# Kernel tuning notes

Measured on AMD Instinct MI355X. Metric: run time of the kernel, lower is better.

The kernel has to match this reference:

```python
import jax, jax.numpy as jnp
import numpy as np

V, E, U, B, S = 32000, 512, 1024, 16, 128
BN_EPS = 1e-3  # keras BatchNormalization default


def setup_inputs() -> dict:
    key = jax.random.key(0)
    ks = jax.random.split(key, 12)
    w = 0.05  # small init keeps the relu-activated LSTM recurrence stable
    return {
        "inputs": jax.random.randint(ks[0], (B, S), 0, V),
        "enc_hidden": jax.random.normal(ks[1], (B, U), jnp.float32) * 0.1,
        "enc_cell": jax.random.normal(ks[2], (B, U), jnp.float32) * 0.1,
        "emb": jax.random.normal(ks[3], (V, E), jnp.float32) * w,
        "Wx": jax.random.normal(ks[4], (E, 4 * U), jnp.float32) * w,
        "Wh": jax.random.normal(ks[5], (U, 4 * U), jnp.float32) * w,
        "b": jnp.zeros((4 * U,), jnp.float32),
        "gamma": jnp.ones((U,), jnp.float32),
        "beta": jnp.zeros((U,), jnp.float32),
        "mov_mean": jnp.zeros((U,), jnp.float32),
        "mov_var": jnp.ones((U,), jnp.float32),
        "W1": jax.random.normal(ks[6], (U, U), jnp.float32) * w,
        "b1": jnp.zeros((U,), jnp.float32),
        "W2": jax.random.normal(ks[7], (U, V), jnp.float32) * w,
        "b2": jnp.zeros((V,), jnp.float32),
    }


def _lstm_relu(xg, mask, h0, c0, Wh):
    # xg: [S,B,4U] precomputed input gates; mask: [S,B] (mask_zero semantics)
    def step(carry, inp):
        h, c = carry
        g, m = inp
        z = g + h @ Wh  # [B,4U]
        i, f, cc, o = jnp.split(z, 4, axis=-1)  # keras gate order i,f,c,o
        i = jax.nn.sigmoid(i)
        f = jax.nn.sigmoid(f)
        o = jax.nn.sigmoid(o)
        cc = jax.nn.relu(cc)  # activation='relu' on candidate
        c_new = f * c + i * cc
        h_new = o * jax.nn.relu(c_new)  # activation='relu' on output
        m = m[:, None]
        h_new = jnp.where(m, h_new, h)  # masked step: carry state/output
        c_new = jnp.where(m, c_new, c)
        return (h_new, c_new), h_new

    (_, _), hs = jax.lax.scan(step, (h0, c0), (xg, mask))
    return hs  # [S,B,U]


def reference(inputs, enc_hidden, enc_cell, emb, Wx, Wh, b, gamma, beta,
              mov_mean, mov_var, W1, b1, W2, b2):
    x = emb[inputs]                       # [B,S,E]
    mask = (inputs != 0)                  # mask_zero=True
    xg = jnp.einsum("bse,eg->bsg", x, Wx) + b   # [B,S,4U]
    hs = _lstm_relu(xg.transpose(1, 0, 2), mask.T, enc_hidden, enc_cell, Wh)
    h = hs.transpose(1, 0, 2)             # [B,S,U]
    # BatchNorm (inference: moving statistics), Dropout is identity at inference
    hbn = (h - mov_mean) * jax.lax.rsqrt(mov_var + BN_EPS) * gamma + beta
    d1 = jax.nn.relu(hbn @ W1 + b1)       # [B,S,U]
    logits = d1 @ W2 + b2                 # [B,S,V]
    return jax.nn.softmax(logits, axis=-1)
```

## Files before the change

kernel.cpp:

```cpp
#include <hip/hip_runtime.h>
#include <hip/hip_bf16.h>
#include <stdint.h>

typedef unsigned short u16;
typedef unsigned int u32;
typedef unsigned long long u64;
typedef __attribute__((ext_vector_type(4))) float f32x4;
typedef __attribute__((ext_vector_type(8))) short s16x8;

#define AT_LD(p)    __hip_atomic_load((p), __ATOMIC_RELAXED, __HIP_MEMORY_SCOPE_AGENT)
#define AT_ST(p, v) __hip_atomic_store((p), (v), __ATOMIC_RELAXED, __HIP_MEMORY_SCOPE_AGENT)


static __device__ __forceinline__ u16 f2bf(float f) {
  union { float f; unsigned u; } v; v.f = f;
  unsigned r = v.u + 0x7FFFu + ((v.u >> 16) & 1u);
  return (u16)(r >> 16);
}

static __device__ __forceinline__ void gload_lds16(const void* g, void* l) {
  __builtin_amdgcn_global_load_lds(
      (const __attribute__((address_space(1))) unsigned int*)(uintptr_t)g,
      (__attribute__((address_space(3))) unsigned int*)(uintptr_t)l,
      16, 0, 0);
}

static __device__ __forceinline__ int swzB(int B) {
  int pos = (B >> 4) & 127;
  int row = (B >> 11) & 15;
  int slot = (pos ^ row ^ (pos >> 3)) & 7;
  int npos = (pos & 0x78) | slot;
  return (B & ~0x7F0) | (npos << 4);
}


__global__ void embed_kernel(const int* __restrict__ inputs,
                             const float* __restrict__ emb,
                             u16* __restrict__ xbf) {
  int i = blockIdx.x * 256 + threadIdx.x;
  int row = i >> 6;
  int e0 = (i & 63) << 3;
  int tok = inputs[row];
  const float* src = emb + (size_t)tok * 512 + e0;
  s16x8 o;
#pragma unroll
  for (int j = 0; j < 8; ++j) o[j] = (short)f2bf(src[j]);
  *(s16x8*)(xbf + (size_t)row * 512 + e0) = o;
}

__global__ void mask_kernel(const int* __restrict__ inputs, u64* __restrict__ mb) {
  int t = threadIdx.x;
  if (t < 32) {
    int b = t >> 1, h = t & 1;
    u64 m = 0;
    for (int j = 0; j < 64; ++j)
      m |= (u64)(inputs[b * 128 + h * 64 + j] != 0) << j;
    mb[t] = m;
  }
}

__global__ void transpose_bf16(const float* __restrict__ W, u16* __restrict__ Wt,
                               int K, int N) {
  __shared__ float t[32][33];
  int ntn = N >> 5;
  int tn = blockIdx.x % ntn, tk = blockIdx.x / ntn;
  int n0 = tn << 5, k0 = tk << 5;
  int tx = threadIdx.x & 31, ty = threadIdx.x >> 5;
#pragma unroll
  for (int j = 0; j < 4; ++j) {
    int k = ty * 4 + j;
    t[k][tx] = W[(size_t)(k0 + k) * N + n0 + tx];
  }
  __syncthreads();
#pragma unroll
  for (int j = 0; j < 4; ++j) {
    int n = ty * 4 + j;
    Wt[(size_t)(n0 + n) * K + k0 + tx] = f2bf(t[tx][n]);
  }
}

template <int MODE>
__global__ __launch_bounds__(256)
void gemm_bf16(const u16* __restrict__ A, const u16* __restrict__ Bt,
               const float* __restrict__ bias, void* __restrict__ Cptr,
               float* __restrict__ rowsum, int M, int N, int K) {
  (void)M;
  __shared__ u16 sA[128 * 32];
  __shared__ u16 sB[128 * 32];
  const int nbn = N >> 7;
  const int nwg = gridDim.x;
  int bid = blockIdx.x;
  int q = nwg >> 3;
  int swz = (bid & 7) * q + (bid >> 3);
  int bm = swz / nbn, bn = swz % nbn;
  const int brow = bm << 7, bcol = bn << 7;

  const int tid = threadIdx.x;
  const int lane = tid & 63;
  const int wv = tid >> 6;
  const int wr = (wv >> 1) * 64, wc = (wv & 1) * 64;
  const int ln = lane & 15, kh = lane >> 4;

  const int srow = tid >> 2;
  const int kch = (tid & 3) << 3;

  f32x4 acc[4][4] = {};

  const int nk = K >> 5;
  const u16* Abase = A + (size_t)(brow + srow) * K + kch;
  const u16* Bbase = Bt + (size_t)(bcol + srow) * K + kch;
  const size_t rstride = (size_t)64 * K;
  u16* lA = sA + srow * 32 + kch;
  u16* lB = sB + srow * 32 + kch;

  for (int kt = 0; kt < nk; ++kt) {
    const int k0 = kt << 5;
    gload_lds16(Abase + k0, lA);
    gload_lds16(Abase + rstride + k0, lA + 64 * 32);
    gload_lds16(Bbase + k0, lB);
    gload_lds16(Bbase + rstride + k0, lB + 64 * 32);
    __syncthreads();
    s16x8 aF[4], bF[4];
#pragma unroll
    for (int m = 0; m < 4; ++m)
      aF[m] = *(const s16x8*)(sA + (wr + m * 16 + ln) * 32 + kh * 8);
#pragma unroll
    for (int n = 0; n < 4; ++n)
      bF[n] = *(const s16x8*)(sB + (wc + n * 16 + ln) * 32 + kh * 8);
#pragma unroll
    for (int m = 0; m < 4; ++m)
#pragma unroll
      for (int n = 0; n < 4; ++n)
        acc[m][n] = __builtin_amdgcn_mfma_f32_16x16x32_bf16(aF[m], bF[n], acc[m][n], 0, 0, 0);
    __syncthreads();
  }

  const int browq = brow + wr;
  const int bcolq = bcol + wc;

  if (MODE == 1) {
    u16* O = (u16*)Cptr;
#pragma unroll
    for (int n = 0; n < 4; ++n) {
      int gcol = bcolq + n * 16 + ln;
      float bv = bias[gcol];
#pragma unroll
      for (int m = 0; m < 4; ++m)
#pragma unroll
        for (int r = 0; r < 4; ++r) {
          int grow = browq + m * 16 + kh * 4 + r;
          float v = fmaxf(acc[m][n][r] + bv, 0.f);
          O[(size_t)grow * N + gcol] = f2bf(v);
        }
    }
  } else {
    float* O = (float*)Cptr;
    float rs[4][4] = {};
#pragma unroll
    for (int n = 0; n < 4; ++n) {
      int gcol = bcolq + n * 16 + ln;
      float bv = bias[gcol];
#pragma unroll
      for (int m = 0; m < 4; ++m)
#pragma unroll
        for (int r = 0; r < 4; ++r) {
          int grow = browq + m * 16 + kh * 4 + r;
          float v = acc[m][n][r] + bv;
          if (MODE == 2) { v = __expf(v); rs[m][r] += v; }
          O[(size_t)grow * N + gcol] = v;
        }
    }
    if (MODE == 2) {
#pragma unroll
      for (int m = 0; m < 4; ++m)
#pragma unroll
        for (int r = 0; r < 4; ++r) {
          float v = rs[m][r];
          v += __shfl_xor(v, 1);
          v += __shfl_xor(v, 2);
          v += __shfl_xor(v, 4);
          v += __shfl_xor(v, 8);
          if (ln == 0) atomicAdd(&rowsum[browq + m * 16 + kh * 4 + r], v);
        }
    }
  }
}

__global__ __launch_bounds__(512, 1)
void lstm_kernel(const float* __restrict__ xg,
                 const u16* __restrict__ Wht,
                 const u64* __restrict__ maskb,
                 const float* __restrict__ ench, const float* __restrict__ encc,
                 const float* __restrict__ gamma, const float* __restrict__ beta,
                 const float* __restrict__ mmean, const float* __restrict__ mvar,
                 u32* __restrict__ hbuf32,
                 u16* __restrict__ hbn,
                 u32* __restrict__ cnt) {
  __shared__ char hA[32 * 1024];
  __shared__ float zxP[8][16][16];

  const int wg = blockIdx.x;
  const int u0 = wg << 4;
  const int tid = threadIdx.x;
  const int lane = tid & 63;
  const int wv = tid >> 6;
  const int ln = lane & 15, khq = lane >> 4;
  const int cg = wv & 3, kh2 = wv >> 2;

  const int g = ln & 3;
  const int unit = u0 + cg * 4 + (ln >> 2);

  s16x8 bW[16];
  {
    const u16* wrow = Wht + (size_t)(g * 1024 + unit) * 1024 + kh2 * 512 + khq * 8;
#pragma unroll
    for (int kt = 0; kt < 16; ++kt)
      bW[kt] = *(const s16x8*)(wrow + kt * 32);
#pragma unroll
    for (int kt = 0; kt < 16; ++kt)
      asm volatile("" : "+v"(bW[kt]));
  }

  float cellR[4] = {}, holdR[4] = {}, xgr[4] = {};
  u64 mA[4] = {}, mB[4] = {};
  float bn_s = 0.f, bn_b = 0.f;
  const size_t bstride = (size_t)128 * 4096;
  const float* xbase = xg + (size_t)(khq * 4) * bstride + g * 1024 + unit;
  if (kh2 == 0) {
    bn_s = gamma[unit] * rsqrtf(mvar[unit] + 1e-3f);
    bn_b = beta[unit] - mmean[unit] * bn_s;
#pragma unroll
    for (int r = 0; r < 4; ++r) {
      int batch = khq * 4 + r;
      cellR[r] = encc[batch * 1024 + unit];
      holdR[r] = ench[batch * 1024 + unit];
      mA[r] = maskb[batch * 2];
      mB[r] = maskb[batch * 2 + 1];
    }
#pragma unroll
    for (int r = 0; r < 4; ++r) {
      u32 w = (u32)f2bf(holdR[r]);
      u32 pw = (u32)__shfl_xor((int)w, 4);
      if ((ln & 7) == 0) {
        int batch = khq * 4 + r;
        AT_ST((u32*)((char*)hbuf32 + batch * 2048 + unit * 2), (w & 0xFFFFu) | (pw << 16));
      }
    }
#pragma unroll
    for (int r = 0; r < 4; ++r) xgr[r] = xbase[r * bstride];
  }
  asm volatile("s_waitcnt vmcnt(0)" ::: "memory");
  __syncthreads();
  if (tid == 0) {
    int oldv = (int)__hip_atomic_fetch_add(cnt, 1, __ATOMIC_RELAXED, __HIP_MEMORY_SCOPE_AGENT);
    if (oldv != 63) {
      int c = 0;
      while (AT_LD((const u32*)cnt) < 64u) { if (++c > (1 << 20)) break; }
    }
  }
  __syncthreads();

  for (int s = 0; s < 128; ++s) {
    u64 st[8];
    {
      const u64* base = (const u64*)((const char*)hbuf32 + (s & 1) * 32768) + tid;
#pragma unroll
      for (int k = 0; k < 8; ++k) {
        const u64* pp = base + k * 512;
        asm volatile("global_load_dwordx2 %0, %1, off sc0 sc1" : "=v"(st[k]) : "v"(pp));
      }
      asm volatile("s_waitcnt vmcnt(0)" ::: "memory");
      __builtin_amdgcn_sched_barrier(0);
#pragma unroll
      for (int k = 0; k < 8; ++k)
        *(u64*)(hA + swzB((tid + k * 512) * 8)) = st[k];
    }
    __syncthreads();

    f32x4 acc0 = {0.f, 0.f, 0.f, 0.f};
    f32x4 acc1 = {0.f, 0.f, 0.f, 0.f};
#pragma unroll
    for (int kt = 0; kt < 16; kt += 2) {
      s16x8 a0 = *(const s16x8*)(hA + swzB(ln * 2048 + kh2 * 1024 + kt * 64 + khq * 16));
      acc0 = __builtin_amdgcn_mfma_f32_16x16x32_bf16(a0, bW[kt], acc0, 0, 0, 0);
      s16x8 a1 = *(const s16x8*)(hA + swzB(ln * 2048 + kh2 * 1024 + (kt + 1) * 64 + khq * 16));
      acc1 = __builtin_amdgcn_mfma_f32_16x16x32_bf16(a1, bW[kt + 1], acc1, 0, 0, 0);
    }
    f32x4 accs = acc0 + acc1;
#pragma unroll
    for (int r = 0; r < 4; ++r) zxP[wv][khq * 4 + r][ln] = accs[r];
    __syncthreads();

    if (kh2 == 0) {
      u16 hbb[4], hbnb[4];
#pragma unroll
      for (int r = 0; r < 4; ++r) {
        int batch = khq * 4 + r;
        float z = zxP[cg][batch][ln] + zxP[cg + 4][batch][ln] + xgr[r];
        float sig = 1.f / (1.f + __expf(-z));
        float val = (g == 2) ? fmaxf(z, 0.f) : sig;
        float v1 = __shfl_xor(val, 1);
        float v2 = __shfl_xor(val, 2);
        float v3 = __shfl_xor(val, 3);
        float cnew = v1 * cellR[r] + val * v2;
        float hnew = v3 * fmaxf(cnew, 0.f);
        u64 mm = (s < 64) ? mA[r] : mB[r];
        if (!((mm >> (s & 63)) & 1)) { cnew = cellR[r]; hnew = holdR[r]; }
        cellR[r] = cnew;
        holdR[r] = hnew;
        hbb[r] = f2bf(hnew);
        hbnb[r] = f2bf(hnew * bn_s + bn_b);
      }
#pragma unroll
      for (int r = 0; r < 4; ++r) {
        u32 w = (u32)hbb[r] | ((u32)hbnb[r] << 16);
        u32 pw = (u32)__shfl_xor((int)w, 4);
        if ((ln & 7) == 0) {
          int batch = khq * 4 + r;
          u32 hpair = (w & 0xFFFFu) | ((pw & 0xFFFFu) << 16);
          u32 bnpair = (w >> 16) | (pw & 0xFFFF0000u);
          if (s < 127) {
            int B = batch * 2048 + unit * 2;
            AT_ST((u32*)((char*)hbuf32 + ((s + 1) & 1) * 32768 + B), hpair);
          }
          *(u32*)((char*)hbn + (size_t)(batch * 128 + s) * 2048 + unit * 2) = bnpair;
        }
      }
    }

    if (s < 127) {
      asm volatile("s_waitcnt vmcnt(0)" ::: "memory");
      __syncthreads();
      int oldv = -1;
      if (tid == 0)
        oldv = (int)__hip_atomic_fetch_add(cnt, 1, __ATOMIC_RELAXED, __HIP_MEMORY_SCOPE_AGENT);
      if (kh2 == 0) {
        const float* xb = xbase + (size_t)(s + 1) * 4096;
#pragma unroll
        for (int r = 0; r < 4; ++r) xgr[r] = xb[r * bstride];
      }
      if (tid == 0) {
        const u32 target = (u32)(s + 2) * 64u;
        if (oldv != (int)target - 1) {
          int c = 0;
          while (AT_LD((const u32*)cnt) < target) { if (++c > (1 << 20)) break; }
        }
      }
      __syncthreads();
    }
  }
}


__global__ void rcp_kernel(float* rs) {
  int i = blockIdx.x * 256 + threadIdx.x;
  rs[i] = 1.0f / rs[i];
}

__global__ void scale_kernel(float* __restrict__ out, const float* __restrict__ rinv) {
  const int total4 = 16384000;
  for (int i = blockIdx.x * 256 + threadIdx.x; i < total4; i += gridDim.x * 256) {
    float4* p = (float4*)out + i;
    float4 v = *p;
    int row = i / 8000;
    float sF = rinv[row];
    v.x *= sF; v.y *= sF; v.z *= sF; v.w *= sF;
    *p = v;
  }
}


extern "C" void kernel_launch(void* const* d_in, const int* in_sizes, int n_in,
                              void* d_out, int out_size, void* d_ws, size_t ws_size,
                              hipStream_t stream) {
  (void)in_sizes; (void)n_in; (void)out_size;
  const int*   inputs = (const int*)d_in[0];
  const float* ench   = (const float*)d_in[1];
  const float* encc   = (const float*)d_in[2];
  const float* emb    = (const float*)d_in[3];
  const float* Wx     = (const float*)d_in[4];
  const float* Wh     = (const float*)d_in[5];
  const float* bb     = (const float*)d_in[6];
  const float* gamma  = (const float*)d_in[7];
  const float* beta   = (const float*)d_in[8];
  const float* mmean  = (const float*)d_in[9];
  const float* mvar   = (const float*)d_in[10];
  const float* W1     = (const float*)d_in[11];
  const float* b1     = (const float*)d_in[12];
  const float* W2     = (const float*)d_in[13];
  const float* b2     = (const float*)d_in[14];
  float* out = (float*)d_out;

  char* p = (char*)d_ws;
  u32*   cnt    = (u32*)(p + 0);
  float* rowsum = (float*)(p + 1024);
  u64*   maskb  = (u64*)(p + 10240);
  u32*   hbuf32 = (u32*)(p + 16384);
  size_t off = 81920;
  u16*   xbf  = (u16*)(p + off);     off += (size_t)2048 * 512 * 2;
  u16*   Wxt  = (u16*)(p + off);     off += (size_t)4096 * 512 * 2;
  u16*   Wht  = (u16*)(p + off);     off += (size_t)4096 * 1024 * 2;
  u16*   W1t  = (u16*)(p + off);     off += (size_t)1024 * 1024 * 2;
  u16*   W2t  = (u16*)(p + off);     off += (size_t)32000 * 1024 * 2;
  float* xg   = (float*)(p + off);   off += (size_t)2048 * 4096 * 4;
  u16*   hbn  = (u16*)(p + off);     off += (size_t)2048 * 1024 * 2;
  u16*   d1   = (u16*)(p + off);     off += (size_t)2048 * 1024 * 2;
  if (ws_size < off) return;

  hipMemsetAsync(d_ws, 0, 9216, stream);

  embed_kernel<<<512, 256, 0, stream>>>(inputs, emb, xbf);
  mask_kernel<<<1, 64, 0, stream>>>(inputs, maskb);
  transpose_bf16<<<(512 / 32) * (4096 / 32), 256, 0, stream>>>(Wx, Wxt, 512, 4096);
  transpose_bf16<<<(1024 / 32) * (4096 / 32), 256, 0, stream>>>(Wh, Wht, 1024, 4096);
  transpose_bf16<<<(1024 / 32) * (1024 / 32), 256, 0, stream>>>(W1, W1t, 1024, 1024);
  transpose_bf16<<<(1024 / 32) * (32000 / 32), 256, 0, stream>>>(W2, W2t, 1024, 32000);

  gemm_bf16<0><<<16 * 32, 256, 0, stream>>>(xbf, Wxt, bb, xg, nullptr, 2048, 4096, 512);

  lstm_kernel<<<64, 512, 0, stream>>>(xg, Wht, maskb, ench, encc, gamma, beta,
                                      mmean, mvar, hbuf32, hbn, cnt);

  gemm_bf16<1><<<16 * 8, 256, 0, stream>>>(hbn, W1t, b1, d1, nullptr, 2048, 1024, 1024);
  gemm_bf16<2><<<16 * 250, 256, 0, stream>>>(d1, W2t, b2, out, rowsum, 2048, 32000, 1024);

  rcp_kernel<<<8, 256, 0, stream>>>(rowsum);
  scale_kernel<<<2048, 256, 0, stream>>>(out, rowsum);
}
```

Measured before the change: 1.003 ms.

## Use hierarchical grid barrier, padded LDS layout, and defer hbn stores in LSTM

Replaces the single global atomic counter barrier in the persistent LSTM kernel with a two-level tree (8 leaf counters on separate cache lines feeding a root counter) and adds s_sleep while spinning, to reduce atomic contention on one address. The h-state staging into LDS switches from 8-byte swizzled stores to 16-byte loads/stores into a padded row layout (2064-byte stride), which removes the swizzle arithmetic. The batch-norm output store is moved after the barrier arrival so it is no longer waited on before signalling. The extra barrier level adds latency to each step, and sleeping may delay wakeup.

After: 1.069 ms. 1.07x slower.

```diff
diff --git a/kernel.cpp b/kernel.cpp
--- a/kernel.cpp
+++ b/kernel.cpp
@@ -7,9 +7,11 @@
 typedef unsigned long long u64;
 typedef __attribute__((ext_vector_type(4))) float f32x4;
 typedef __attribute__((ext_vector_type(8))) short s16x8;
+typedef __attribute__((ext_vector_type(4))) unsigned int u32x4;
 
 #define AT_LD(p)    __hip_atomic_load((p), __ATOMIC_RELAXED, __HIP_MEMORY_SCOPE_AGENT)
 #define AT_ST(p, v) __hip_atomic_store((p), (v), __ATOMIC_RELAXED, __HIP_MEMORY_SCOPE_AGENT)
+#define AT_FAA(p)   __hip_atomic_fetch_add((p), 1u, __ATOMIC_RELAXED, __HIP_MEMORY_SCOPE_AGENT)
 
 
 static __device__ __forceinline__ u16 f2bf(float f) {
@@ -23,14 +25,6 @@
       (const __attribute__((address_space(1))) unsigned int*)(uintptr_t)g,
       (__attribute__((address_space(3))) unsigned int*)(uintptr_t)l,
       16, 0, 0);
-}
-
-static __device__ __forceinline__ int swzB(int B) {
-  int pos = (B >> 4) & 127;
-  int row = (B >> 11) & 15;
-  int slot = (pos ^ row ^ (pos >> 3)) & 7;
-  int npos = (pos & 0x78) | slot;
-  return (B & ~0x7F0) | (npos << 4);
 }
 
 
@@ -195,8 +189,8 @@
                  const float* __restrict__ mmean, const float* __restrict__ mvar,
                  u32* __restrict__ hbuf32,
                  u16* __restrict__ hbn,
-                 u32* __restrict__ cnt) {
-  __shared__ char hA[32 * 1024];
+                 u32* __restrict__ sync) {
+  __shared__ char hA[16 * 2064];
   __shared__ float zxP[8][16][16];
 
   const int wg = blockIdx.x;
@@ -209,6 +203,9 @@
 
   const int g = ln & 3;
   const int unit = u0 + cg * 4 + (ln >> 2);
+
+  u32* leaf = sync + (wg >> 3) * 64;
+  u32* root = sync + 512;
 
   s16x8 bW[16];
   {
@@ -251,46 +248,63 @@
   }
   asm volatile("s_waitcnt vmcnt(0)" ::: "memory");
   __syncthreads();
+  int syncno = 1;
   if (tid == 0) {
-    int oldv = (int)__hip_atomic_fetch_add(cnt, 1, __ATOMIC_RELAXED, __HIP_MEMORY_SCOPE_AGENT);
-    if (oldv != 63) {
+    bool last = false;
+    u32 lo = AT_FAA(leaf);
+    if (lo == (u32)(syncno * 8 - 1)) {
+      u32 ro = AT_FAA(root);
+      last = (ro == (u32)(syncno * 8 - 1));
+    }
+    if (!last) {
       int c = 0;
-      while (AT_LD((const u32*)cnt) < 64u) { if (++c > (1 << 20)) break; }
+      while (AT_LD(root) < (u32)(syncno * 8)) {
+        __builtin_amdgcn_s_sleep(1);
+        if (++c > (1 << 18)) break;
+      }
     }
   }
   __syncthreads();
 
   for (int s = 0; s < 128; ++s) {
-    u64 st[8];
     {
-      const u64* base = (const u64*)((const char*)hbuf32 + (s & 1) * 32768) + tid;
-#pragma unroll
-      for (int k = 0; k < 8; ++k) {
-        const u64* pp = base + k * 512;
-        asm volatile("global_load_dwordx2 %0, %1, off sc0 sc1" : "=v"(st[k]) : "v"(pp));
+      u32x4 st[4];
+      const char* base = (const char*)hbuf32 + (s & 1) * 32768 + tid * 16;
+#pragma unroll
+      for (int k = 0; k < 4; ++k) {
+        const char* pp = base + k * 8192;
+        asm volatile("global_load_dwordx4 %0, %1, off sc0 sc1" : "=v"(st[k]) : "v"(pp));
       }
       asm volatile("s_waitcnt vmcnt(0)" ::: "memory");
       __builtin_amdgcn_sched_barrier(0);
 #pragma unroll
-      for (int k = 0; k < 8; ++k)
-        *(u64*)(hA + swzB((tid + k * 512) * 8)) = st[k];
+      for (int k = 0; k < 4; ++k) {
+        int idx = tid + k * 512;
+        int row = idx >> 7;
+        int col = (idx & 127) * 16;
+        *(u32x4*)(hA + row * 2064 + col) = st[k];
+      }
     }
     __syncthreads();
 
     f32x4 acc0 = {0.f, 0.f, 0.f, 0.f};
     f32x4 acc1 = {0.f, 0.f, 0.f, 0.f};
-#pragma unroll
-    for (int kt = 0; kt < 16; kt += 2) {
-      s16x8 a0 = *(const s16x8*)(hA + swzB(ln * 2048 + kh2 * 1024 + kt * 64 + khq * 16));
-      acc0 = __builtin_amdgcn_mfma_f32_16x16x32_bf16(a0, bW[kt], acc0, 0, 0, 0);
-      s16x8 a1 = *(const s16x8*)(hA + swzB(ln * 2048 + kh2 * 1024 + (kt + 1) * 64 + khq * 16));
-      acc1 = __builtin_amdgcn_mfma_f32_16x16x32_bf16(a1, bW[kt + 1], acc1, 0, 0, 0);
+    {
+      const char* arow = hA + ln * 2064 + kh2 * 1024 + khq * 16;
+#pragma unroll
+      for (int kt = 0; kt < 16; kt += 2) {
+        s16x8 a0 = *(const s16x8*)(arow + kt * 64);
+        acc0 = __builtin_amdgcn_mfma_f32_16x16x32_bf16(a0, bW[kt], acc0, 0, 0, 0);
+        s16x8 a1 = *(const s16x8*)(arow + (kt + 1) * 64);
+        acc1 = __builtin_amdgcn_mfma_f32_16x16x32_bf16(a1, bW[kt + 1], acc1, 0, 0, 0);
+      }
     }
     f32x4 accs = acc0 + acc1;
 #pragma unroll
     for (int r = 0; r < 4; ++r) zxP[wv][khq * 4 + r][ln] = accs[r];
     __syncthreads();
 
+    u32 bnpair[4];
     if (kh2 == 0) {
       u16 hbb[4], hbnb[4];
 #pragma unroll
@@ -315,15 +329,11 @@
       for (int r = 0; r < 4; ++r) {
         u32 w = (u32)hbb[r] | ((u32)hbnb[r] << 16);
         u32 pw = (u32)__shfl_xor((int)w, 4);
-        if ((ln & 7) == 0) {
+        u32 hpair = (w & 0xFFFFu) | ((pw & 0xFFFFu) << 16);
+        bnpair[r] = (w >> 16) | (pw & 0xFFFF0000u);
+        if (s < 127 && (ln & 7) == 0) {
           int batch = khq * 4 + r;
-          u32 hpair = (w & 0xFFFFu) | ((pw & 0xFFFFu) << 16);
-          u32 bnpair = (w >> 16) | (pw & 0xFFFF0000u);
-          if (s < 127) {
-            int B = batch * 2048 + unit * 2;
-            AT_ST((u32*)((char*)hbuf32 + ((s + 1) & 1) * 32768 + B), hpair);
-          }
-          *(u32*)((char*)hbn + (size_t)(batch * 128 + s) * 2048 + unit * 2) = bnpair;
+          AT_ST((u32*)((char*)hbuf32 + ((s + 1) & 1) * 32768 + batch * 2048 + unit * 2), hpair);
         }
       }
     }
@@ -331,22 +341,41 @@
     if (s < 127) {
       asm volatile("s_waitcnt vmcnt(0)" ::: "memory");
       __syncthreads();
-      int oldv = -1;
-      if (tid == 0)
-        oldv = (int)__hip_atomic_fetch_add(cnt, 1, __ATOMIC_RELAXED, __HIP_MEMORY_SCOPE_AGENT);
+      ++syncno;
+      bool last = false;
+      if (tid == 0) {
+        u32 lo = AT_FAA(leaf);
+        if (lo == (u32)(syncno * 8 - 1)) {
+          u32 ro = AT_FAA(root);
+          last = (ro == (u32)(syncno * 8 - 1));
+        }
+      }
       if (kh2 == 0) {
+        if ((ln & 7) == 0) {
+#pragma unroll
+          for (int r = 0; r < 4; ++r) {
+            int batch = khq * 4 + r;
+            *(u32*)((char*)hbn + (size_t)(batch * 128 + s) * 2048 + unit * 2) = bnpair[r];
+          }
+        }
         const float* xb = xbase + (size_t)(s + 1) * 4096;
 #pragma unroll
         for (int r = 0; r < 4; ++r) xgr[r] = xb[r * bstride];
       }
-      if (tid == 0) {
-        const u32 target = (u32)(s + 2) * 64u;
-        if (oldv != (int)target - 1) {
-          int c = 0;
-          while (AT_LD((const u32*)cnt) < target) { if (++c > (1 << 20)) break; }
+      if (tid == 0 && !last) {
+        int c = 0;
+        while (AT_LD(root) < (u32)(syncno * 8)) {
+          __builtin_amdgcn_s_sleep(1);
+          if (++c > (1 << 18)) break;
         }
       }
       __syncthreads();
+    } else if (kh2 == 0 && (ln & 7) == 0) {
+#pragma unroll
+      for (int r = 0; r < 4; ++r) {
+        int batch = khq * 4 + r;
+        *(u32*)((char*)hbn + (size_t)(batch * 128 + s) * 2048 + unit * 2) = bnpair[r];
+      }
     }
   }
 }
@@ -392,9 +421,9 @@
   float* out = (float*)d_out;
 
   char* p = (char*)d_ws;
-  u32*   cnt    = (u32*)(p + 0);
-  float* rowsum = (float*)(p + 1024);
-  u64*   maskb  = (u64*)(p + 10240);
+  u32*   sync   = (u32*)(p + 0);
+  float* rowsum = (float*)(p + 4096);
+  u64*   maskb  = (u64*)(p + 12288);
   u32*   hbuf32 = (u32*)(p + 16384);
   size_t off = 81920;
   u16*   xbf  = (u16*)(p + off);     off += (size_t)2048 * 512 * 2;
@@ -407,7 +436,7 @@
   u16*   d1   = (u16*)(p + off);     off += (size_t)2048 * 1024 * 2;
   if (ws_size < off) return;
 
-  hipMemsetAsync(d_ws, 0, 9216, stream);
+  hipMemsetAsync(d_ws, 0, 16384, stream);
 
   embed_kernel<<<512, 256, 0, stream>>>(inputs, emb, xbf);
   mask_kernel<<<1, 64, 0, stream>>>(inputs, maskb);
@@ -419,7 +448,7 @@
   gemm_bf16<0><<<16 * 32, 256, 0, stream>>>(xbf, Wxt, bb, xg, nullptr, 2048, 4096, 512);
 
   lstm_kernel<<<64, 512, 0, stream>>>(xg, Wht, maskb, ench, encc, gamma, beta,
-                                      mmean, mvar, hbuf32, hbn, cnt);
+                                      mmean, mvar, hbuf32, hbn, sync);
 
   gemm_bf16<1><<<16 * 8, 256, 0, stream>>>(hbn, W1t, b1, d1, nullptr, 2048, 1024, 1024);
   gemm_bf16<2><<<16 * 250, 256, 0, stream>>>(d1, W2t, b2, out, rowsum, 2048, 32000, 1024);
```

## Halve LSTM grid by giving each wave full K range, drop LDS partial-sum reduction

Applied to the files above, without the earlier changes.

The persistent LSTM kernel now runs on 32 workgroups, each covering 32 units. Each wave holds the full 1024-wide K slice of Wh in registers (32 bf16 fragments) instead of splitting K across two wave halves, which removes the zxP LDS reduction and one __syncthreads per step. The hbn stores are deferred until after the barrier arrive, spin-waits gain s_sleep, and the rcp kernel is folded into scale_kernel. The trade-off is higher register pressure, twice the MFMA chain per wave, and fewer CUs doing the recurrence, in exchange for fewer grid-barrier participants and less intra-step sync.

Measured after the change: 978.5 us. -2.4%, faster.

```diff
diff --git a/kernel.cpp b/kernel.cpp
--- a/kernel.cpp
+++ b/kernel.cpp
@@ -10,6 +10,7 @@
 
 #define AT_LD(p)    __hip_atomic_load((p), __ATOMIC_RELAXED, __HIP_MEMORY_SCOPE_AGENT)
 #define AT_ST(p, v) __hip_atomic_store((p), (v), __ATOMIC_RELAXED, __HIP_MEMORY_SCOPE_AGENT)
+#define AT_FAA(p)   __hip_atomic_fetch_add((p), 1u, __ATOMIC_RELAXED, __HIP_MEMORY_SCOPE_AGENT)
 
 
 static __device__ __forceinline__ u16 f2bf(float f) {
@@ -197,65 +198,63 @@
                  u16* __restrict__ hbn,
                  u32* __restrict__ cnt) {
   __shared__ char hA[32 * 1024];
-  __shared__ float zxP[8][16][16];
 
   const int wg = blockIdx.x;
-  const int u0 = wg << 4;
+  const int u0 = wg << 5;
   const int tid = threadIdx.x;
   const int lane = tid & 63;
   const int wv = tid >> 6;
   const int ln = lane & 15, khq = lane >> 4;
-  const int cg = wv & 3, kh2 = wv >> 2;
 
   const int g = ln & 3;
-  const int unit = u0 + cg * 4 + (ln >> 2);
-
-  s16x8 bW[16];
+  const int unit = u0 + wv * 4 + (ln >> 2);
+
+  s16x8 bW[32];
   {
-    const u16* wrow = Wht + (size_t)(g * 1024 + unit) * 1024 + kh2 * 512 + khq * 8;
-#pragma unroll
-    for (int kt = 0; kt < 16; ++kt)
+    const u16* wrow = Wht + (size_t)(g * 1024 + unit) * 1024 + khq * 8;
+#pragma unroll
+    for (int kt = 0; kt < 32; ++kt)
       bW[kt] = *(const s16x8*)(wrow + kt * 32);
 #pragma unroll
-    for (int kt = 0; kt < 16; ++kt)
+    for (int kt = 0; kt < 32; ++kt)
       asm volatile("" : "+v"(bW[kt]));
   }
 
-  float cellR[4] = {}, holdR[4] = {}, xgr[4] = {};
-  u64 mA[4] = {}, mB[4] = {};
-  float bn_s = 0.f, bn_b = 0.f;
+  float cellR[4], holdR[4], xgr[4];
+  u64 mA[4], mB[4];
+  const float bn_s = gamma[unit] * rsqrtf(mvar[unit] + 1e-3f);
+  const float bn_b = beta[unit] - mmean[unit] * bn_s;
   const size_t bstride = (size_t)128 * 4096;
   const float* xbase = xg + (size_t)(khq * 4) * bstride + g * 1024 + unit;
-  if (kh2 == 0) {
-    bn_s = gamma[unit] * rsqrtf(mvar[unit] + 1e-3f);
-    bn_b = beta[unit] - mmean[unit] * bn_s;
-#pragma unroll
-    for (int r = 0; r < 4; ++r) {
+#pragma unroll
+  for (int r = 0; r < 4; ++r) {
+    int batch = khq * 4 + r;
+    cellR[r] = encc[batch * 1024 + unit];
+    holdR[r] = ench[batch * 1024 + unit];
+    mA[r] = maskb[batch * 2];
+    mB[r] = maskb[batch * 2 + 1];
+  }
+#pragma unroll
+  for (int r = 0; r < 4; ++r) {
+    u32 w = (u32)f2bf(holdR[r]);
+    u32 pw = (u32)__shfl_xor((int)w, 4);
+    if ((ln & 7) == 0) {
       int batch = khq * 4 + r;
-      cellR[r] = encc[batch * 1024 + unit];
-      holdR[r] = ench[batch * 1024 + unit];
-      mA[r] = maskb[batch * 2];
-      mB[r] = maskb[batch * 2 + 1];
-    }
-#pragma unroll
-    for (int r = 0; r < 4; ++r) {
-      u32 w = (u32)f2bf(holdR[r]);
-      u32 pw = (u32)__shfl_xor((int)w, 4);
-      if ((ln & 7) == 0) {
-        int batch = khq * 4 + r;
-        AT_ST((u32*)((char*)hbuf32 + batch * 2048 + unit * 2), (w & 0xFFFFu) | (pw << 16));
-      }
-    }
-#pragma unroll
-    for (int r = 0; r < 4; ++r) xgr[r] = xbase[r * bstride];
-  }
+      AT_ST((u32*)((char*)hbuf32 + batch * 2048 + unit * 2), (w & 0xFFFFu) | (pw << 16));
+    }
+  }
+#pragma unroll
+  for (int r = 0; r < 4; ++r) xgr[r] = xbase[r * bstride];
   asm volatile("s_waitcnt vmcnt(0)" ::: "memory");
   __syncthreads();
   if (tid == 0) {
-    int oldv = (int)__hip_atomic_fetch_add(cnt, 1, __ATOMIC_RELAXED, __HIP_MEMORY_SCOPE_AGENT);
-    if (oldv != 63) {
+    u32 oldv = AT_FAA(cnt);
+    if (oldv != 31u) {
       int c = 0;
-      while (AT_LD((const u32*)cnt) < 64u) { if (++c > (1 << 20)) break; }
+      while (AT_LD((const u32*)cnt) < 32u) {
+        __builtin_amdgcn_s_sleep(1);
+        if (++c > (1 << 18)) break;
+      }
     }
   }
   __syncthreads();
@@ -280,23 +279,20 @@
     f32x4 acc0 = {0.f, 0.f, 0.f, 0.f};
     f32x4 acc1 = {0.f, 0.f, 0.f, 0.f};
 #pragma unroll
-    for (int kt = 0; kt < 16; kt += 2) {
-      s16x8 a0 = *(const s16x8*)(hA + swzB(ln * 2048 + kh2 * 1024 + kt * 64 + khq * 16));
+    for (int kt = 0; kt < 32; kt += 2) {
+      s16x8 a0 = *(const s16x8*)(hA + swzB(ln * 2048 + kt * 64 + khq * 16));
       acc0 = __builtin_amdgcn_mfma_f32_16x16x32_bf16(a0, bW[kt], acc0, 0, 0, 0);
-      s16x8 a1 = *(const s16x8*)(hA + swzB(ln * 2048 + kh2 * 1024 + (kt + 1) * 64 + khq * 16));
+      s16x8 a1 = *(const s16x8*)(hA + swzB(ln * 2048 + (kt + 1) * 64 + khq * 16));
       acc1 = __builtin_amdgcn_mfma_f32_16x16x32_bf16(a1, bW[kt + 1], acc1, 0, 0, 0);
     }
     f32x4 accs = acc0 + acc1;
-#pragma unroll
-    for (int r = 0; r < 4; ++r) zxP[wv][khq * 4 + r][ln] = accs[r];
-    __syncthreads();
-
-    if (kh2 == 0) {
+
+    u32 bnpair[4];
+    {
       u16 hbb[4], hbnb[4];
 #pragma unroll
       for (int r = 0; r < 4; ++r) {
-        int batch = khq * 4 + r;
-        float z = zxP[cg][batch][ln] + zxP[cg + 4][batch][ln] + xgr[r];
+        float z = accs[r] + xgr[r];
         float sig = 1.f / (1.f + __expf(-z));
         float val = (g == 2) ? fmaxf(z, 0.f) : sig;
         float v1 = __shfl_xor(val, 1);
@@ -315,15 +311,11 @@
       for (int r = 0; r < 4; ++r) {
         u32 w = (u32)hbb[r] | ((u32)hbnb[r] << 16);
         u32 pw = (u32)__shfl_xor((int)w, 4);
-        if ((ln & 7) == 0) {
+        u32 hpair = (w & 0xFFFFu) | ((pw & 0xFFFFu) << 16);
+        bnpair[r] = (w >> 16) | (pw & 0xFFFF0000u);
+        if (s < 127 && (ln & 7) == 0) {
           int batch = khq * 4 + r;
-          u32 hpair = (w & 0xFFFFu) | ((pw & 0xFFFFu) << 16);
-          u32 bnpair = (w >> 16) | (pw & 0xFFFF0000u);
-          if (s < 127) {
-            int B = batch * 2048 + unit * 2;
-            AT_ST((u32*)((char*)hbuf32 + ((s + 1) & 1) * 32768 + B), hpair);
-          }
-          *(u32*)((char*)hbn + (size_t)(batch * 128 + s) * 2048 + unit * 2) = bnpair;
+          AT_ST((u32*)((char*)hbuf32 + ((s + 1) & 1) * 32768 + batch * 2048 + unit * 2), hpair);
         }
       }
     }
@@ -331,39 +323,49 @@
     if (s < 127) {
       asm volatile("s_waitcnt vmcnt(0)" ::: "memory");
       __syncthreads();
-      int oldv = -1;
-      if (tid == 0)
-        oldv = (int)__hip_atomic_fetch_add(cnt, 1, __ATOMIC_RELAXED, __HIP_MEMORY_SCOPE_AGENT);
-      if (kh2 == 0) {
+      u32 oldv = 0xFFFFFFFFu;
+      if (tid == 0) oldv = AT_FAA(cnt);
+      if ((ln & 7) == 0) {
+#pragma unroll
+        for (int r = 0; r < 4; ++r) {
+          int batch = khq * 4 + r;
+          *(u32*)((char*)hbn + (size_t)(batch * 128 + s) * 2048 + unit * 2) = bnpair[r];
+        }
+      }
+      {
         const float* xb = xbase + (size_t)(s + 1) * 4096;
 #pragma unroll
         for (int r = 0; r < 4; ++r) xgr[r] = xb[r * bstride];
       }
       if (tid == 0) {
-        const u32 target = (u32)(s + 2) * 64u;
-        if (oldv != (int)target - 1) {
+        const u32 target = (u32)(s + 2) * 32u;
+        if (oldv != target - 1u) {
           int c = 0;
-          while (AT_LD((const u32*)cnt) < target) { if (++c > (1 << 20)) break; }
+          while (AT_LD((const u32*)cnt) < target) {
+            __builtin_amdgcn_s_sleep(1);
+            if (++c > (1 << 18)) break;
+          }
         }
       }
       __syncthreads();
-    }
-  }
-}
-
-
-__global__ void rcp_kernel(float* rs) {
-  int i = blockIdx.x * 256 + threadIdx.x;
-  rs[i] = 1.0f / rs[i];
-}
-
-__global__ void scale_kernel(float* __restrict__ out, const float* __restrict__ rinv) {
+    } else if ((ln & 7) == 0) {
+#pragma unroll
+      for (int r = 0; r < 4; ++r) {
+        int batch = khq * 4 + r;
+        *(u32*)((char*)hbn + (size_t)(batch * 128 + s) * 2048 + unit * 2) = bnpair[r];
+      }
+    }
+  }
+}
+
+
+__global__ void scale_kernel(float* __restrict__ out, const float* __restrict__ rs) {
   const int total4 = 16384000;
   for (int i = blockIdx.x * 256 + threadIdx.x; i < total4; i += gridDim.x * 256) {
     float4* p = (float4*)out + i;
     float4 v = *p;
     int row = i / 8000;
-    float sF = rinv[row];
+    float sF = 1.0f / rs[row];
     v.x *= sF; v.y *= sF; v.z *= sF; v.w *= sF;
     *p = v;
   }
@@ -418,12 +420,11 @@
 
   gemm_bf16<0><<<16 * 32, 256, 0, stream>>>(xbf, Wxt, bb, xg, nullptr, 2048, 4096, 512);
 
-  lstm_kernel<<<64, 512, 0, stream>>>(xg, Wht, maskb, ench, encc, gamma, beta,
+  lstm_kernel<<<32, 512, 0, stream>>>(xg, Wht, maskb, ench, encc, gamma, beta,
                                       mmean, mvar, hbuf32, hbn, cnt);
 
   gemm_bf16<1><<<16 * 8, 256, 0, stream>>>(hbn, W1t, b1, d1, nullptr, 2048, 1024, 1024);
   gemm_bf16<2><<<16 * 250, 256, 0, stream>>>(d1, W2t, b2, out, rowsum, 2048, 32000, 1024);
 
-  rcp_kernel<<<8, 256, 0, stream>>>(rowsum);
   scale_kernel<<<2048, 256, 0, stream>>>(out, rowsum);
 }
```
